# Kernel optimization log

Hardware: AMD Instinct MI355X
Metric: run time of the kernel (lower is better)

The kernel has to match this reference:

```python
import jax, jax.numpy as jnp
import numpy as np

HEADS = 8
DIM_HEAD = 128
LN_EPS = 1e-5


def setup_inputs() -> dict:
    key = jax.random.key(0)
    ks = jax.random.split(key, 4)
    N, M, C, V, T = 64, 2, 64, 15, 256
    dim = C * V              # 960
    inner = HEADS * DIM_HEAD # 1024
    return {
        "x": jax.random.normal(ks[0], (N, M, C, V, T), dtype=jnp.float32),
        "ln_g": jnp.ones((dim,), jnp.float32),
        "ln_b": jnp.zeros((dim,), jnp.float32),
        "w_qkv": jax.random.normal(ks[1], (dim, 3 * inner), dtype=jnp.float32) * (dim ** -0.5),
        "w_out": jax.random.normal(ks[2], (inner, dim), dtype=jnp.float32) * (inner ** -0.5),
        "b_out": jnp.zeros((dim,), jnp.float32),
        "w_lin": jax.random.normal(ks[3], (T, T), dtype=jnp.float32) * (T ** -0.5),
        "b_lin": jnp.zeros((T,), jnp.float32),
    }


def reference(x, ln_g, ln_b, w_qkv, w_out, b_out, w_lin, b_lin):
    N, M, C, V, T = x.shape
    dim = C * V
    # [N, M, C, V, T] -> [N*M, T, C*V]
    xs = jnp.transpose(x, (0, 1, 4, 2, 3)).reshape(N * M, T, dim)

    # PreNorm (LayerNorm over last dim)
    mu = jnp.mean(xs, axis=-1, keepdims=True)
    var = jnp.mean(jnp.square(xs - mu), axis=-1, keepdims=True)
    xn = (xs - mu) * jax.lax.rsqrt(var + LN_EPS) * ln_g + ln_b

    # Attention
    qkv = xn @ w_qkv  # [NM, T, 3*inner]
    q, k, v = jnp.split(qkv, 3, axis=-1)
    def to_heads(t):
        return jnp.transpose(t.reshape(N * M, T, HEADS, DIM_HEAD), (0, 2, 1, 3))
    q, k, v = to_heads(q), to_heads(k), to_heads(v)  # [NM, H, T, D]
    scale = DIM_HEAD ** -0.5
    dots = jnp.einsum('nhid,nhjd->nhij', q, k) * scale
    attn = jax.nn.softmax(dots, axis=-1)
    out = jnp.einsum('nhij,nhjd->nhid', attn, v)
    out = jnp.transpose(out, (0, 2, 1, 3)).reshape(N * M, T, HEADS * DIM_HEAD)
    out = out @ w_out + b_out

    # Residual
    xs = out + xs

    # back to [N, M, C, V, T], then Linear over T + tanh
    x2 = jnp.transpose(xs.reshape(N, M, T, C, V), (0, 1, 3, 4, 2))
    y = jnp.tanh(x2 @ w_lin.T + b_lin)
    return y
```

## Files before the change

kernel.cpp:

```cpp
#include <hip/hip_runtime.h>

typedef unsigned short ushort;
using short8 = __attribute__((ext_vector_type(8))) short;
using f32x4  = __attribute__((ext_vector_type(4))) float;
using i32x4  = __attribute__((ext_vector_type(4))) int;
using us4    = __attribute__((ext_vector_type(4))) ushort;

static __device__ __forceinline__ float bf2f(ushort u) {
  union { unsigned int i; float f; } x; x.i = ((unsigned int)u) << 16; return x.f;
}
static __device__ __forceinline__ ushort f2bf(float f) {
  union { float f; unsigned int i; } x; x.f = f;
  unsigned int u = x.i;
  unsigned int r = u + 0x7fffu + ((u >> 16) & 1u);
  return (ushort)(r >> 16);
}

#define GLOAD16(gp, lp)                                                   \
  __builtin_amdgcn_global_load_lds(                                      \
      (const __attribute__((address_space(1))) void*)(gp),               \
      (__attribute__((address_space(3))) void*)(lp), 16, 0, 0)

__global__ __launch_bounds__(256) void wtrans_kernel(const float* __restrict__ in,
                                                     ushort* __restrict__ out,
                                                     int R, int C) {
  __shared__ float sl[32][33];
  int tx = threadIdx.x & 31, ty = threadIdx.x >> 5;
  int c0 = blockIdx.x * 32, r0 = blockIdx.y * 32;
#pragma unroll
  for (int s = 0; s < 4; s++) {
    int r = r0 + ty + s * 8;
    int c = c0 + tx;
    sl[ty + s * 8][tx] = (c < C) ? in[(size_t)r * C + c] : 0.f;
  }
  __syncthreads();
#pragma unroll
  for (int s = 0; s < 4; s++) {
    int c = c0 + ty + s * 8;
    int r = r0 + tx;
    out[(size_t)c * R + r] = f2bf(sl[tx][ty + s * 8]);
  }
}

__global__ void wsplit_kernel(const float* __restrict__ in, ushort* __restrict__ hi,
                              ushort* __restrict__ lo, int n) {
  int i = blockIdx.x * 256 + threadIdx.x;
  if (i < n) {
    float v = in[i];
    ushort h = f2bf(v);
    hi[i] = h;
    lo[i] = f2bf(v - bf2f(h));
  }
}

__global__ __launch_bounds__(512) void ln_fused_kernel(const float* __restrict__ x,
                                                       const float* __restrict__ g,
                                                       const float* __restrict__ b,
                                                       ushort* __restrict__ xn) {
  __shared__ float sl[960][34];
  __shared__ float smean[32], srstd[32];
  int tid = threadIdx.x;
  int nm = blockIdx.y;
  int t0 = blockIdx.x * 32;

  int r0 = tid >> 3, c4 = (tid & 7) * 4;
#pragma unroll
  for (int it = 0; it < 15; it++) {
    int r = it * 64 + r0;
    float4 v = *(const float4*)&x[((size_t)nm * 960 + r) * 256 + t0 + c4];
    *(float4*)&sl[r][c4] = v;
  }
  __syncthreads();

  int tg = tid >> 4, lt = tid & 15;
  float s = 0.f, ss = 0.f;
#pragma unroll 4
  for (int k = 0; k < 60; k++) {
    float v = sl[lt + k * 16][tg];
    s += v; ss += v * v;
  }
#pragma unroll
  for (int d = 1; d < 16; d <<= 1) {
    s += __shfl_xor(s, d, 64);
    ss += __shfl_xor(ss, d, 64);
  }
  if (lt == 0) {
    float mean = s * (1.f / 960.f);
    float var = ss * (1.f / 960.f) - mean * mean;
    smean[tg] = mean;
    srstd[tg] = rsqrtf(var + 1e-5f);
  }
  __syncthreads();

  float gg[2], bb[2];
#pragma unroll
  for (int c = 0; c < 2; c++) {
    int col = c * 512 + tid;
    if (col < 960) { gg[c] = g[col]; bb[c] = b[col]; }
  }
#pragma unroll
  for (int t = 0; t < 32; t++) {
    float mean = smean[t], rstd = srstd[t];
#pragma unroll
    for (int c = 0; c < 2; c++) {
      int col = c * 512 + tid;
      if (col < 960)
        xn[((size_t)nm * 256 + t0 + t) * 960 + col] =
            f2bf((sl[col][t] - mean) * rstd * gg[c] + bb[c]);
    }
  }
}

template <int MODE>
__global__ __launch_bounds__(512, 2) void gemm256(
    const ushort* __restrict__ A, int lda, const ushort* __restrict__ BT, int ldb, int nkt,
    const ushort* __restrict__ Alo, const ushort* __restrict__ Blo,
    ushort* __restrict__ o0, ushort* __restrict__ o1, ushort* __restrict__ o2,
    const float* __restrict__ bias, const float* __restrict__ xres,
    float* __restrict__ fout) {
  __shared__ char smem[131072];
  int tid = threadIdx.x;
  int l = tid & 63, w = tid >> 6;
  int wr = w >> 2, wc = w & 3;
  int lr = l & 15, lg = l >> 4;
  int cb = blockIdx.x * 256, rb = blockIdx.y * 256;

  int srow = tid >> 2;
  int scol = ((tid & 3) ^ ((tid >> 3) & 3)) * 8;

  int swz = (lg ^ ((lr >> 1) & 3)) << 4;
  const char* ArdB = smem + (wr * 128 + lr) * 64 + swz;
  const char* BrdB = smem + 65536 + (wc * 64 + lr) * 64 + swz;

  auto stage_half = [&](int kt, int kk, int isB) {
    const ushort* P; int ld; int k0;
    if (MODE == 2) {
      int seg = kt >> 2; k0 = (kt & 3) * 64 + kk * 32;
      P = isB ? ((seg == 1) ? Blo : BT) : ((seg == 2) ? Alo : A);
      ld = 256;
    } else {
      P = isB ? BT : A; ld = isB ? ldb : lda; k0 = kt * 64 + kk * 32;
    }
    const ushort* gp = P + (size_t)((isB ? cb : rb) + srow) * ld + k0 + scol;
    char* dst = smem + isB * 65536 + (kt & 1) * 32768 + kk * 16384 + tid * 16;
    GLOAD16(gp, dst);
    GLOAD16(gp + (size_t)128 * ld, dst + 8192);
  };

  f32x4 acc[8][4];
#pragma unroll
  for (int i = 0; i < 8; i++)
#pragma unroll
    for (int j = 0; j < 4; j++) acc[i][j] = (f32x4){0.f, 0.f, 0.f, 0.f};

  stage_half(0, 0, 0); stage_half(0, 0, 1); stage_half(0, 1, 0); stage_half(0, 1, 1);
  asm volatile("s_waitcnt vmcnt(4)" ::: "memory");
  __builtin_amdgcn_s_barrier();

  for (int t = 0; t < nkt; t++) {
    const char* Ard = ArdB + (t & 1) * 32768;
    const char* Brd = BrdB + (t & 1) * 32768;
    bool st = (t + 1 < nkt);
    short8 a[4], b[4];

#pragma unroll
    for (int j = 0; j < 4; j++) b[j] = *(const short8*)(Brd + j * 1024);
#pragma unroll
    for (int i = 0; i < 4; i++) a[i] = *(const short8*)(Ard + i * 1024);
    if (st) stage_half(t + 1, 0, 0);
    __builtin_amdgcn_s_barrier();
    __builtin_amdgcn_s_setprio(1);
#pragma unroll
    for (int i = 0; i < 4; i++)
#pragma unroll
      for (int j = 0; j < 4; j++)
        acc[i][j] = __builtin_amdgcn_mfma_f32_16x16x32_bf16(a[i], b[j], acc[i][j], 0, 0, 0);
    __builtin_amdgcn_s_setprio(0);
    __builtin_amdgcn_s_barrier();

#pragma unroll
    for (int i = 0; i < 4; i++) a[i] = *(const short8*)(Ard + (4 + i) * 1024);
    if (st) stage_half(t + 1, 0, 1);
    __builtin_amdgcn_s_barrier();
    __builtin_amdgcn_s_setprio(1);
#pragma unroll
    for (int i = 0; i < 4; i++)
#pragma unroll
      for (int j = 0; j < 4; j++)
        acc[4 + i][j] = __builtin_amdgcn_mfma_f32_16x16x32_bf16(a[i], b[j], acc[4 + i][j], 0, 0, 0);
    __builtin_amdgcn_s_setprio(0);
    if (st) asm volatile("s_waitcnt vmcnt(4)" ::: "memory");
    else    asm volatile("s_waitcnt vmcnt(0)" ::: "memory");
    __builtin_amdgcn_s_barrier();

#pragma unroll
    for (int j = 0; j < 4; j++) b[j] = *(const short8*)(Brd + 16384 + j * 1024);
#pragma unroll
    for (int i = 0; i < 4; i++) a[i] = *(const short8*)(Ard + 16384 + i * 1024);
    if (st) stage_half(t + 1, 1, 0);
    __builtin_amdgcn_s_barrier();
    __builtin_amdgcn_s_setprio(1);
#pragma unroll
    for (int i = 0; i < 4; i++)
#pragma unroll
      for (int j = 0; j < 4; j++)
        acc[i][j] = __builtin_amdgcn_mfma_f32_16x16x32_bf16(a[i], b[j], acc[i][j], 0, 0, 0);
    __builtin_amdgcn_s_setprio(0);
    __builtin_amdgcn_s_barrier();

#pragma unroll
    for (int i = 0; i < 4; i++) a[i] = *(const short8*)(Ard + 16384 + (4 + i) * 1024);
    if (st) stage_half(t + 1, 1, 1);
    __builtin_amdgcn_s_barrier();
    __builtin_amdgcn_s_setprio(1);
#pragma unroll
    for (int i = 0; i < 4; i++)
#pragma unroll
      for (int j = 0; j < 4; j++)
        acc[4 + i][j] = __builtin_amdgcn_mfma_f32_16x16x32_bf16(a[i], b[j], acc[4 + i][j], 0, 0, 0);
    __builtin_amdgcn_s_setprio(0);
    if (st) asm volatile("s_waitcnt vmcnt(4)" ::: "memory");
    else    asm volatile("s_waitcnt vmcnt(0)" ::: "memory");
    __builtin_amdgcn_s_barrier();
  }

  int row0 = rb + wr * 128, col0 = cb + wc * 64;
  if (MODE == 0) {
    int nm = rb >> 8;
    int which = cb >> 10;
#pragma unroll
    for (int i = 0; i < 8; i++)
#pragma unroll
      for (int j = 0; j < 4; j++) {
        f32x4 v = acc[i][j];
        int col = col0 + j * 16 + lr;
        int cl = col & 1023;
        int h = cl >> 7, d = cl & 127;
        int nmh = nm * 8 + h;
        int t0 = wr * 128 + i * 16 + lg * 4;
        if (which == 2) {
          us4 pk;
          pk.x = f2bf(v[0]); pk.y = f2bf(v[1]); pk.z = f2bf(v[2]); pk.w = f2bf(v[3]);
          *(us4*)&o2[((size_t)nmh * 128 + d) * 256 + t0] = pk;
        } else if (which == 0) {
#pragma unroll
          for (int r = 0; r < 4; r++)
            o0[((size_t)nmh * 256 + t0 + r) * 128 + d] = f2bf(v[r] * 0.08838834764831845f);
        } else {
#pragma unroll
          for (int r = 0; r < 4; r++)
            o1[((size_t)nmh * 256 + t0 + r) * 128 + d] = f2bf(v[r]);
        }
      }
  } else if (MODE == 1) {
    int nm = rb >> 8;
#pragma unroll
    for (int i = 0; i < 8; i++)
#pragma unroll
      for (int j = 0; j < 4; j++) {
        f32x4 v = acc[i][j];
        int cvl = wc * 64 + j * 16 + lr;
        int col = cb + cvl;
        float bb = (col < 960) ? bias[col] : 0.f;
        int t0 = wr * 128 + i * 16 + lg * 4;
        us4 pk;
        pk.x = f2bf(v[0] + bb); pk.y = f2bf(v[1] + bb);
        pk.z = f2bf(v[2] + bb); pk.w = f2bf(v[3] + bb);
        *(us4*)(smem + cvl * 512 + ((t0 * 2) ^ ((cvl & 15) << 3))) = pk;
      }
    __syncthreads();
    for (int it = 0; it < 32; it++) {
      int cvl = it * 8 + w;
      int col = cb + cvl;
      if (col < 960) {
        us4 pv = *(const us4*)(smem + cvl * 512 + ((l * 8) ^ ((cvl & 15) << 3)));
        size_t base = ((size_t)nm * 960 + col) * 256 + l * 4;
        f32x4 xv = *(const f32x4*)&xres[base];
        us4 h4, l4;
#pragma unroll
        for (int e = 0; e < 4; e++) {
          float s = xv[e] + bf2f(pv[e]);
          ushort hh = f2bf(s);
          h4[e] = hh;
          l4[e] = f2bf(s - bf2f(hh));
        }
        *(us4*)&o0[base] = h4;
        *(us4*)&o1[base] = l4;
      }
    }
  } else {
#pragma unroll
    for (int i = 0; i < 8; i++)
#pragma unroll
      for (int j = 0; j < 4; j++) {
        f32x4 v = acc[i][j];
        int col = col0 + j * 16 + lr;
        float bb = bias[col];
#pragma unroll
        for (int r = 0; r < 4; r++) {
          int row = row0 + i * 16 + lg * 4 + r;
          fout[(size_t)row * 256 + col] = tanhf(v[r] + bb);
        }
      }
  }
}

__global__ __launch_bounds__(512, 2) void attn2_kernel(const ushort* __restrict__ q,
                                                       const ushort* __restrict__ kb,
                                                       const ushort* __restrict__ vT,
                                                       ushort* __restrict__ ao) {
  __shared__ char smem[131072];
  int tid = threadIdx.x;
  int l = tid & 63, w = tid >> 6;
  int lr = l & 15, lg = l >> 4;
  int nmh = blockIdx.x;

  const ushort* kbase = kb + (size_t)nmh * 32768;
  const ushort* vbase = vT + (size_t)nmh * 32768;

#pragma unroll
  for (int u = 0; u < 8; u++) {
    int row = u * 32 + w * 4 + (l >> 4);
    int slot = l & 15;
    GLOAD16(kbase + row * 128 + ((slot ^ (row & 7)) * 8), smem + u * 8192 + w * 1024);
  }
  short8 aq[2][4];
  {
    const ushort* qp = q + (size_t)nmh * 32768 + (size_t)(w * 32 + lr) * 128 + lg * 8;
#pragma unroll
    for (int i = 0; i < 2; i++)
#pragma unroll
      for (int kk = 0; kk < 4; kk++) aq[i][kk] = *(const short8*)(qp + i * 2048 + kk * 32);
  }
#pragma unroll
  for (int u = 0; u < 8; u++) {
    int row = u * 16 + w * 2 + (l >> 5);
    int slot = l & 31;
    GLOAD16(vbase + row * 256 + ((slot ^ (row & 7)) * 8),
            smem + 65536 + u * 8192 + w * 1024);
  }
  asm volatile("s_waitcnt vmcnt(8)" ::: "memory");
  __builtin_amdgcn_s_barrier();

  f32x4 s_acc[2][16];
#pragma unroll
  for (int i = 0; i < 2; i++)
#pragma unroll
    for (int j = 0; j < 16; j++) s_acc[i][j] = (f32x4){0.f, 0.f, 0.f, 0.f};
#pragma unroll
  for (int j = 0; j < 16; j++) {
    short8 bk[4];
#pragma unroll
    for (int kk = 0; kk < 4; kk++)
      bk[kk] = *(const short8*)(smem + (j * 16 + lr) * 256 + (((kk * 4 + lg) ^ (lr & 7)) << 4));
#pragma unroll
    for (int i = 0; i < 2; i++)
#pragma unroll
      for (int kk = 0; kk < 4; kk++)
        s_acc[i][j] = __builtin_amdgcn_mfma_f32_16x16x32_bf16(aq[i][kk], bk[kk], s_acc[i][j], 0, 0, 0);
  }

  float m[2][4], sum[2][4], rs[2][4];
#pragma unroll
  for (int i = 0; i < 2; i++)
#pragma unroll
    for (int r = 0; r < 4; r++) m[i][r] = -1e30f;
#pragma unroll
  for (int i = 0; i < 2; i++)
#pragma unroll
    for (int j = 0; j < 16; j++)
#pragma unroll
      for (int r = 0; r < 4; r++) m[i][r] = fmaxf(m[i][r], s_acc[i][j][r]);
#pragma unroll
  for (int d = 1; d < 16; d <<= 1)
#pragma unroll
    for (int i = 0; i < 2; i++)
#pragma unroll
      for (int r = 0; r < 4; r++) m[i][r] = fmaxf(m[i][r], __shfl_xor(m[i][r], d, 64));
#pragma unroll
  for (int i = 0; i < 2; i++)
#pragma unroll
    for (int r = 0; r < 4; r++) sum[i][r] = 0.f;
#pragma unroll
  for (int i = 0; i < 2; i++)
#pragma unroll
    for (int j = 0; j < 16; j++)
#pragma unroll
      for (int r = 0; r < 4; r++) {
        float p = __expf(s_acc[i][j][r] - m[i][r]);
        s_acc[i][j][r] = p;
        sum[i][r] += p;
      }
#pragma unroll
  for (int d = 1; d < 16; d <<= 1)
#pragma unroll
    for (int i = 0; i < 2; i++)
#pragma unroll
      for (int r = 0; r < 4; r++) sum[i][r] += __shfl_xor(sum[i][r], d, 64);
#pragma unroll
  for (int i = 0; i < 2; i++)
#pragma unroll
    for (int r = 0; r < 4; r++) rs[i][r] = 1.f / sum[i][r];

  __builtin_amdgcn_s_barrier();
  asm volatile("s_waitcnt vmcnt(0)" ::: "memory");

  char* Pb = smem + w * 4608;
  f32x4 o_acc[2][8];
#pragma unroll
  for (int i = 0; i < 2; i++)
#pragma unroll
    for (int j = 0; j < 8; j++) o_acc[i][j] = (f32x4){0.f, 0.f, 0.f, 0.f};

#pragma unroll
  for (int ct = 0; ct < 4; ct++) {
#pragma unroll
    for (int i = 0; i < 2; i++)
#pragma unroll
      for (int jj = 0; jj < 4; jj++)
#pragma unroll
        for (int r = 0; r < 4; r++)
          *(ushort*)(Pb + (i * 16 + lg * 4 + r) * 144 + (jj * 16 + lr) * 2) =
              f2bf(s_acc[i][ct * 4 + jj][r]);
    short8 pa[2][2];
#pragma unroll
    for (int i = 0; i < 2; i++)
#pragma unroll
      for (int kk = 0; kk < 2; kk++)
        pa[i][kk] = *(const short8*)(Pb + (i * 16 + lr) * 144 + kk * 64 + lg * 16);
#pragma unroll
    for (int j = 0; j < 8; j++) {
      short8 bv[2];
#pragma unroll
      for (int kk = 0; kk < 2; kk++)
        bv[kk] = *(const short8*)(smem + 65536 + (j * 16 + lr) * 512 +
                                  (((ct * 8 + kk * 4 + lg) ^ (lr & 7)) << 4));
#pragma unroll
      for (int i = 0; i < 2; i++)
#pragma unroll
        for (int kk = 0; kk < 2; kk++)
          o_acc[i][j] = __builtin_amdgcn_mfma_f32_16x16x32_bf16(pa[i][kk], bv[kk], o_acc[i][j], 0, 0, 0);
    }
  }

  int nm = nmh >> 3, h = nmh & 7;
#pragma unroll
  for (int i = 0; i < 2; i++)
#pragma unroll
    for (int j = 0; j < 8; j++)
#pragma unroll
      for (int r = 0; r < 4; r++) {
        int t = w * 32 + i * 16 + lg * 4 + r;
        int d = h * 128 + j * 16 + lr;
        ao[((size_t)nm * 256 + t) * 1024 + d] = f2bf(o_acc[i][j][r] * rs[i][r]);
      }
}

extern "C" void kernel_launch(void* const* d_in, const int* in_sizes, int n_in,
                              void* d_out, int out_size, void* d_ws, size_t ws_size,
                              hipStream_t stream) {
  const float* x = (const float*)d_in[0];
  const float* ln_g = (const float*)d_in[1];
  const float* ln_b = (const float*)d_in[2];
  const float* w_qkv = (const float*)d_in[3];
  const float* w_out = (const float*)d_in[4];
  const float* b_out = (const float*)d_in[5];
  const float* w_lin = (const float*)d_in[6];
  const float* b_lin = (const float*)d_in[7];
  float* out = (float*)d_out;

  char* ws = (char*)d_ws;
  size_t off = 0;
  auto alloc = [&](size_t bytes) -> void* {
    void* p = ws + off;
    off = (off + bytes + 255) & ~(size_t)255;
    return p;
  };

  ushort* wqkvT = (ushort*)alloc((size_t)3072 * 960 * 2);
  ushort* woutT = (ushort*)alloc((size_t)1024 * 1024 * 2);
  ushort* whi   = (ushort*)alloc((size_t)65536 * 2);
  ushort* wlo   = (ushort*)alloc((size_t)65536 * 2);
  ushort* xn    = (ushort*)alloc((size_t)32768 * 960 * 2);
  ushort* qbuf  = (ushort*)alloc((size_t)1024 * 256 * 128 * 2);
  ushort* kbuf  = (ushort*)alloc((size_t)1024 * 256 * 128 * 2);
  ushort* vTbuf = (ushort*)alloc((size_t)1024 * 256 * 128 * 2);
  ushort* attnout = (ushort*)alloc((size_t)32768 * 1024 * 2);
  ushort* x2hi  = kbuf;
  ushort* x2lo  = vTbuf;

  wtrans_kernel<<<dim3(96, 30), 256, 0, stream>>>(w_qkv, wqkvT, 960, 3072);
  wtrans_kernel<<<dim3(32, 32), 256, 0, stream>>>(w_out, woutT, 1024, 960);
  wsplit_kernel<<<dim3(256), 256, 0, stream>>>(w_lin, whi, wlo, 65536);

  ln_fused_kernel<<<dim3(8, 128), 512, 0, stream>>>(x, ln_g, ln_b, xn);

  gemm256<0><<<dim3(12, 128), 512, 0, stream>>>(xn, 960, wqkvT, 960, 15, nullptr, nullptr,
                                                qbuf, kbuf, vTbuf, nullptr, nullptr, nullptr);
  attn2_kernel<<<dim3(1024), 512, 0, stream>>>(qbuf, kbuf, vTbuf, attnout);
  gemm256<1><<<dim3(4, 128), 512, 0, stream>>>(attnout, 1024, woutT, 1024, 16, nullptr, nullptr,
                                               x2hi, x2lo, nullptr, b_out, x, nullptr);
  gemm256<2><<<dim3(1, 480), 512, 0, stream>>>(x2hi, 256, whi, 256, 12, x2lo, wlo,
                                               nullptr, nullptr, nullptr, b_lin, nullptr, out);
}
```

Baseline: 592.6 us.

## Fuse residual add and hi/lo split into final linear+tanh kernel

The out-projection GEMM now writes a transposed bf16 projection with bias straight to global memory, with no LDS transpose or residual step. A new final kernel loads x and that projection, forms the residual sum, and splits it into bf16 hi/lo in LDS. It then runs the three-term split-precision GEMM over T with tanh. This drops the x2hi/x2lo global round trip and the separate mode-2 GEMM. The cost is a final GEMM that reads B fragments directly from global without LDS staging or pipelining, and uncoalesced scalar output stores.

```diff
diff --git a/kernel.cpp b/kernel.cpp
--- a/kernel.cpp
+++ b/kernel.cpp
@@ -114,10 +114,8 @@
 template <int MODE>
 __global__ __launch_bounds__(512, 2) void gemm256(
     const ushort* __restrict__ A, int lda, const ushort* __restrict__ BT, int ldb, int nkt,
-    const ushort* __restrict__ Alo, const ushort* __restrict__ Blo,
     ushort* __restrict__ o0, ushort* __restrict__ o1, ushort* __restrict__ o2,
-    const float* __restrict__ bias, const float* __restrict__ xres,
-    float* __restrict__ fout) {
+    const float* __restrict__ bias) {
   __shared__ char smem[131072];
   int tid = threadIdx.x;
   int l = tid & 63, w = tid >> 6;
@@ -133,14 +131,9 @@
   const char* BrdB = smem + 65536 + (wc * 64 + lr) * 64 + swz;
 
   auto stage_half = [&](int kt, int kk, int isB) {
-    const ushort* P; int ld; int k0;
-    if (MODE == 2) {
-      int seg = kt >> 2; k0 = (kt & 3) * 64 + kk * 32;
-      P = isB ? ((seg == 1) ? Blo : BT) : ((seg == 2) ? Alo : A);
-      ld = 256;
-    } else {
-      P = isB ? BT : A; ld = isB ? ldb : lda; k0 = kt * 64 + kk * 32;
-    }
+    const ushort* P = isB ? BT : A;
+    int ld = isB ? ldb : lda;
+    int k0 = kt * 64 + kk * 32;
     const ushort* gp = P + (size_t)((isB ? cb : rb) + srow) * ld + k0 + scol;
     char* dst = smem + isB * 65536 + (kt & 1) * 32768 + kk * 16384 + tid * 16;
     GLOAD16(gp, dst);
@@ -224,7 +217,7 @@
     __builtin_amdgcn_s_barrier();
   }
 
-  int row0 = rb + wr * 128, col0 = cb + wc * 64;
+  int col0 = cb + wc * 64;
   if (MODE == 0) {
     int nm = rb >> 8;
     int which = cb >> 10;
@@ -252,55 +245,20 @@
             o1[((size_t)nmh * 256 + t0 + r) * 128 + d] = f2bf(v[r]);
         }
       }
-  } else if (MODE == 1) {
+  } else {
     int nm = rb >> 8;
 #pragma unroll
     for (int i = 0; i < 8; i++)
 #pragma unroll
       for (int j = 0; j < 4; j++) {
         f32x4 v = acc[i][j];
-        int cvl = wc * 64 + j * 16 + lr;
-        int col = cb + cvl;
+        int col = col0 + j * 16 + lr;
         float bb = (col < 960) ? bias[col] : 0.f;
         int t0 = wr * 128 + i * 16 + lg * 4;
         us4 pk;
         pk.x = f2bf(v[0] + bb); pk.y = f2bf(v[1] + bb);
         pk.z = f2bf(v[2] + bb); pk.w = f2bf(v[3] + bb);
-        *(us4*)(smem + cvl * 512 + ((t0 * 2) ^ ((cvl & 15) << 3))) = pk;
-      }
-    __syncthreads();
-    for (int it = 0; it < 32; it++) {
-      int cvl = it * 8 + w;
-      int col = cb + cvl;
-      if (col < 960) {
-        us4 pv = *(const us4*)(smem + cvl * 512 + ((l * 8) ^ ((cvl & 15) << 3)));
-        size_t base = ((size_t)nm * 960 + col) * 256 + l * 4;
-        f32x4 xv = *(const f32x4*)&xres[base];
-        us4 h4, l4;
-#pragma unroll
-        for (int e = 0; e < 4; e++) {
-          float s = xv[e] + bf2f(pv[e]);
-          ushort hh = f2bf(s);
-          h4[e] = hh;
-          l4[e] = f2bf(s - bf2f(hh));
-        }
-        *(us4*)&o0[base] = h4;
-        *(us4*)&o1[base] = l4;
-      }
-    }
-  } else {
-#pragma unroll
-    for (int i = 0; i < 8; i++)
-#pragma unroll
-      for (int j = 0; j < 4; j++) {
-        f32x4 v = acc[i][j];
-        int col = col0 + j * 16 + lr;
-        float bb = bias[col];
-#pragma unroll
-        for (int r = 0; r < 4; r++) {
-          int row = row0 + i * 16 + lg * 4 + r;
-          fout[(size_t)row * 256 + col] = tanhf(v[r] + bb);
-        }
+        *(us4*)&o0[((size_t)nm * 1024 + col) * 256 + t0] = pk;
       }
   }
 }
@@ -454,6 +412,89 @@
         int d = h * 128 + j * 16 + lr;
         ao[((size_t)nm * 256 + t) * 1024 + d] = f2bf(o_acc[i][j][r] * rs[i][r]);
       }
+}
+
+__global__ __launch_bounds__(512, 2) void ffinal_kernel(
+    const float* __restrict__ x, const ushort* __restrict__ projT,
+    const ushort* __restrict__ whi, const ushort* __restrict__ wlo,
+    const float* __restrict__ blin, float* __restrict__ out) {
+  __shared__ char sm[98304];
+  int tid = threadIdx.x;
+  int l = tid & 63, w = tid >> 6;
+  int lr = l & 15, lg = l >> 4;
+  int cv0 = blockIdx.x * 96;
+  int nm = blockIdx.y;
+
+  int rloc = tid >> 4;
+  int tseg = (tid & 15) * 16;
+#pragma unroll
+  for (int ps = 0; ps < 3; ps++) {
+    int row = ps * 32 + rloc;
+    size_t gbase = ((size_t)nm * 960 + cv0 + row) * 256 + tseg;
+    size_t pbase = ((size_t)nm * 1024 + cv0 + row) * 256 + tseg;
+    int sw = (row & 31) << 4;
+#pragma unroll
+    for (int c = 0; c < 4; c++) {
+      f32x4 xv = *(const f32x4*)&x[gbase + c * 4];
+      us4 pv = *(const us4*)&projT[pbase + c * 4];
+      us4 h4, l4;
+#pragma unroll
+      for (int e = 0; e < 4; e++) {
+        float s = xv[e] + bf2f(pv[e]);
+        ushort hh = f2bf(s);
+        h4[e] = hh;
+        l4[e] = f2bf(s - bf2f(hh));
+      }
+      int tb = (tseg + c * 4) * 2;
+      *(us4*)(sm + row * 512 + (tb ^ sw)) = h4;
+      *(us4*)(sm + 49152 + row * 512 + (tb ^ sw)) = l4;
+    }
+  }
+  __syncthreads();
+
+  int wr3 = w >> 2, wc3 = w & 3;
+  f32x4 acc[3][4];
+#pragma unroll
+  for (int i = 0; i < 3; i++)
+#pragma unroll
+    for (int j = 0; j < 4; j++) acc[i][j] = (f32x4){0.f, 0.f, 0.f, 0.f};
+
+#pragma unroll
+  for (int kt = 0; kt < 24; kt++) {
+    int seg = kt >> 3;
+    int k32 = (kt & 7) * 32;
+    const ushort* B = (seg == 1) ? wlo : whi;
+    int aoff = (seg == 2) ? 49152 : 0;
+    short8 bf[4];
+#pragma unroll
+    for (int nj = 0; nj < 4; nj++)
+      bf[nj] = *(const short8*)&B[(wc3 * 64 + nj * 16 + lr) * 256 + k32 + lg * 8];
+    short8 af[3];
+#pragma unroll
+    for (int i = 0; i < 3; i++) {
+      int row = wr3 * 48 + i * 16 + lr;
+      int tb = (k32 + lg * 8) * 2;
+      af[i] = *(const short8*)(sm + aoff + row * 512 + (tb ^ ((row & 31) << 4)));
+    }
+#pragma unroll
+    for (int i = 0; i < 3; i++)
+#pragma unroll
+      for (int nj = 0; nj < 4; nj++)
+        acc[i][nj] = __builtin_amdgcn_mfma_f32_16x16x32_bf16(af[i], bf[nj], acc[i][nj], 0, 0, 0);
+  }
+
+#pragma unroll
+  for (int i = 0; i < 3; i++)
+#pragma unroll
+    for (int nj = 0; nj < 4; nj++) {
+      int tout = wc3 * 64 + nj * 16 + lr;
+      float bb = blin[tout];
+#pragma unroll
+      for (int r = 0; r < 4; r++) {
+        int cv = cv0 + wr3 * 48 + i * 16 + lg * 4 + r;
+        out[((size_t)nm * 960 + cv) * 256 + tout] = tanhf(acc[i][nj][r] + bb);
+      }
+    }
 }
 
 extern "C" void kernel_launch(void* const* d_in, const int* in_sizes, int n_in,
@@ -486,8 +527,7 @@
   ushort* kbuf  = (ushort*)alloc((size_t)1024 * 256 * 128 * 2);
   ushort* vTbuf = (ushort*)alloc((size_t)1024 * 256 * 128 * 2);
   ushort* attnout = (ushort*)alloc((size_t)32768 * 1024 * 2);
-  ushort* x2hi  = kbuf;
-  ushort* x2lo  = vTbuf;
+  ushort* projT = qbuf;
 
   wtrans_kernel<<<dim3(96, 30), 256, 0, stream>>>(w_qkv, wqkvT, 960, 3072);
   wtrans_kernel<<<dim3(32, 32), 256, 0, stream>>>(w_out, woutT, 1024, 960);
@@ -495,11 +535,10 @@
 
   ln_fused_kernel<<<dim3(8, 128), 512, 0, stream>>>(x, ln_g, ln_b, xn);
 
-  gemm256<0><<<dim3(12, 128), 512, 0, stream>>>(xn, 960, wqkvT, 960, 15, nullptr, nullptr,
-                                                qbuf, kbuf, vTbuf, nullptr, nullptr, nullptr);
+  gemm256<0><<<dim3(12, 128), 512, 0, stream>>>(xn, 960, wqkvT, 960, 15,
+                                                qbuf, kbuf, vTbuf, nullptr);
   attn2_kernel<<<dim3(1024), 512, 0, stream>>>(qbuf, kbuf, vTbuf, attnout);
-  gemm256<1><<<dim3(4, 128), 512, 0, stream>>>(attnout, 1024, woutT, 1024, 16, nullptr, nullptr,
-                                               x2hi, x2lo, nullptr, b_out, x, nullptr);
-  gemm256<2><<<dim3(1, 480), 512, 0, stream>>>(x2hi, 256, whi, 256, 12, x2lo, wlo,
-                                               nullptr, nullptr, nullptr, b_lin, nullptr, out);
-}
+  gemm256<1><<<dim3(4, 128), 512, 0, stream>>>(attnout, 1024, woutT, 1024, 16,
+                                               projT, nullptr, nullptr, b_out);
+  ffinal_kernel<<<dim3(10, 128), 512, 0, stream>>>(x, projT, whi, wlo, b_lin, out);
+}
```

Result: slower. 671.5 us (+13.3%).
